# Performance work log

Hardware: AMD Instinct MI355X
Metric: run time of the kernel (lower is better)

The kernel has to match this reference:

```python
import jax, jax.numpy as jnp
import numpy as np

N = 2
GRIDS = [(512, 512), (256, 256), (128, 128), (64, 64), (32, 32)]
STRIDES = [4, 8, 16, 32, 64]
SIZES = [32, 64, 128, 256, 512]
ASPECTS = (0.5, 1.0, 2.0)
A = len(ASPECTS)
IMG_H = IMG_W = 2048
PRE_NMS = 1000      # pre_nms_top_n['testing']
POST_NMS = 1000     # post_nms_top_n['testing']
NMS_THRESH = 0.7
SCORE_THRESH = 0.0
MIN_SIZE = 1e-3
BBOX_XFORM_CLIP = float(np.log(1000.0 / 16.0))  # torchvision BoxCoder clamp


def _make_anchors():
    """AnchorGenerator.grid_anchors for each level; returns list of [H*W*A, 4]."""
    ar = jnp.asarray(ASPECTS, jnp.float32)
    hr = jnp.sqrt(ar)
    wr = 1.0 / hr
    levels = []
    for (gh, gw), s, size in zip(GRIDS, STRIDES, SIZES):
        ws = wr * size
        hs = hr * size
        base = jnp.round(jnp.stack([-ws, -hs, ws, hs], 1) / 2.0)  # [A,4]
        sx = (jnp.arange(gw) * s).astype(jnp.float32)
        sy = (jnp.arange(gh) * s).astype(jnp.float32)
        yy, xx = jnp.meshgrid(sy, sx, indexing='ij')
        shifts = jnp.stack([xx.ravel(), yy.ravel(), xx.ravel(), yy.ravel()], 1)
        levels.append((shifts[:, None, :] + base[None, :, :]).reshape(-1, 4))
    return levels


def _flatten_obj(o):
    # permute_and_flatten with C=1: [N,A,H,W] -> [N, H*W*A]
    n, ac, h, w = o.shape
    return o.reshape(n, ac, 1, h, w).transpose(0, 3, 4, 1, 2).reshape(n, -1)


def _flatten_box(b):
    # permute_and_flatten with C=4: [N,A*4,H,W] -> [N, H*W*A, 4]
    n, a4, h, w = b.shape
    return b.reshape(n, a4 // 4, 4, h, w).transpose(0, 3, 4, 1, 2).reshape(n, -1, 4)


def _decode(deltas, anchors):
    # BoxCoder.decode with weights (1,1,1,1); deltas [N,M,4], anchors [M,4]
    wa = anchors[:, 2] - anchors[:, 0]
    ha = anchors[:, 3] - anchors[:, 1]
    cxa = anchors[:, 0] + 0.5 * wa
    cya = anchors[:, 1] + 0.5 * ha
    dx, dy = deltas[..., 0], deltas[..., 1]
    dw = jnp.minimum(deltas[..., 2], BBOX_XFORM_CLIP)
    dh = jnp.minimum(deltas[..., 3], BBOX_XFORM_CLIP)
    cx = dx * wa + cxa
    cy = dy * ha + cya
    w = jnp.exp(dw) * wa
    h = jnp.exp(dh) * ha
    return jnp.stack([cx - 0.5 * w, cy - 0.5 * h, cx + 0.5 * w, cy + 0.5 * h], -1)


def _nms_select(boxes, scores, n_out, thresh):
    """Greedy NMS returning fixed n_out (index, valid) pairs. boxes [K,4]."""
    area = jnp.maximum(boxes[:, 2] - boxes[:, 0], 0.0) * jnp.maximum(boxes[:, 3] - boxes[:, 1], 0.0)

    def step(s, _):
        i = jnp.argmax(s)
        valid = s[i] > -jnp.inf
        b = boxes[i]
        lt = jnp.maximum(boxes[:, :2], b[:2])
        rb = jnp.minimum(boxes[:, 2:], b[2:])
        wh = jnp.maximum(rb - lt, 0.0)
        inter = wh[:, 0] * wh[:, 1]
        iou = inter / (area + area[i] - inter + 1e-9)
        s = jnp.where(iou > thresh, -jnp.inf, s).at[i].set(-jnp.inf)
        return s, (i, valid)

    _, (idx, valid) = jax.lax.scan(step, scores, None, length=n_out)
    return idx, valid


def _rpn_forward(objs, dts):
    anchors = _make_anchors()
    b_all, s_all, l_all = [], [], []
    for li, (o, d, a) in enumerate(zip(objs, dts, anchors)):
        of = _flatten_obj(o)            # [N, HWA]
        df = _flatten_box(d)            # [N, HWA, 4]
        props = _decode(df, a)          # [N, HWA, 4]
        k = min(PRE_NMS, of.shape[1])
        ts, ti = jax.lax.top_k(of, k)   # top-k on raw objectness (per level)
        b_all.append(jnp.take_along_axis(props, ti[..., None], 1))
        s_all.append(ts)
        l_all.append(jnp.full((of.shape[0], k), float(li), jnp.float32))
    boxes = jnp.concatenate(b_all, 1)   # [N, K, 4]
    raw = jnp.concatenate(s_all, 1)     # [N, K]
    lvl = jnp.concatenate(l_all, 1)     # [N, K]

    def per_image(bx, rs, lv):
        sc = jax.nn.sigmoid(rs)
        x1 = jnp.clip(bx[:, 0], 0.0, IMG_W)
        y1 = jnp.clip(bx[:, 1], 0.0, IMG_H)
        x2 = jnp.clip(bx[:, 2], 0.0, IMG_W)
        y2 = jnp.clip(bx[:, 3], 0.0, IMG_H)
        bx = jnp.stack([x1, y1, x2, y2], 1)
        keep = ((x2 - x1) >= MIN_SIZE) & ((y2 - y1) >= MIN_SIZE) & (sc > SCORE_THRESH)
        ms = jnp.where(keep, sc, -jnp.inf)
        off = lv * (IMG_W + IMG_H + 1.0)  # batched_nms level offset
        idx, valid = _nms_select(jax.lax.stop_gradient(bx + off[:, None]),
                                 jax.lax.stop_gradient(ms), POST_NMS, NMS_THRESH)
        v = valid.astype(bx.dtype)
        ob = bx[idx] * v[:, None]
        os = sc[idx] * v
        return jnp.concatenate([ob, os[:, None]], 1)  # [POST_NMS, 5]

    return jax.vmap(per_image)(boxes, raw, lvl)       # [N, POST_NMS, 5]


def setup_inputs() -> dict:
    key = jax.random.key(0)
    ks = jax.random.split(key, 10)
    inp = {}
    for i, (gh, gw) in enumerate(GRIDS):
        inp[f"obj{i}"] = jax.random.normal(ks[i], (N, A, gh, gw), jnp.float32)
        inp[f"box{i}"] = jax.random.normal(ks[5 + i], (N, A * 4, gh, gw), jnp.float32) * 0.5
    return inp


def reference(obj0, obj1, obj2, obj3, obj4, box0, box1, box2, box3, box4):
    return _rpn_forward([obj0, obj1, obj2, obj3, obj4],
                        [box0, box1, box2, box3, box4])
```

## Files before the change

kernel.cpp:

```cpp
#include <hip/hip_runtime.h>
#include <cmath>

#pragma clang fp contract(off)

typedef unsigned int u32;
typedef unsigned short u16;
typedef unsigned long long u64;

#define K_PER_LVL 1000
#define KTOT 5000
#define NIMG 2
#define BINS 16384
#define BIN_SHIFT 18
#define SEGW (BINS / 256)
#define EQ_CAP 2048
#define ECAP 32768
#define LECAP 24576
#define CBUF 1024
#define RNK_IB 512
#define RNK_JB 250
#define RNK_NJ (KTOT / RNK_JB)

__constant__ int c_LG[5] = {512, 256, 128, 64, 32};
__constant__ int c_LS[5] = {4, 8, 16, 32, 64};
__constant__ int c_LZ[5] = {32, 64, 128, 256, 512};
__constant__ int c_LM[5] = {786432, 196608, 49152, 12288, 3072};

struct Ptrs { const float* o[5]; const float* b[5]; };

__device__ inline u32 fkey(float f) {
    u32 u = __float_as_uint(f);
    return (u & 0x80000000u) ? ~u : (u | 0x80000000u);
}

__global__ __launch_bounds__(256) void k_zero(u32* __restrict__ z, int nwords) {
    int i = blockIdx.x * 256 + threadIdx.x;
    int stride = gridDim.x * 256;
    for (; i < nwords; i += stride) z[i] = 0;
}

__global__ __launch_bounds__(256) void k_hist(Ptrs P, u32* __restrict__ hist) {
    int p = blockIdx.y; int l = p % 5; int n = p / 5;
    int M4 = c_LM[l] >> 2;
    const float4* base = (const float4*)(P.o[l] + (size_t)n * c_LM[l]);
    __shared__ u32 lh[BINS];
    for (int i = threadIdx.x; i < BINS; i += 256) lh[i] = 0;
    __syncthreads();
    int stride = gridDim.x * 256;
    for (int i = blockIdx.x * 256 + threadIdx.x; i < M4; i += stride) {
        float4 v = base[i];
        atomicAdd(&lh[fkey(v.x) >> BIN_SHIFT], 1u);
        atomicAdd(&lh[fkey(v.y) >> BIN_SHIFT], 1u);
        atomicAdd(&lh[fkey(v.z) >> BIN_SHIFT], 1u);
        atomicAdd(&lh[fkey(v.w) >> BIN_SHIFT], 1u);
    }
    __syncthreads();
    for (int i = threadIdx.x; i < BINS; i += 256) {
        u32 c = lh[i];
        if (c) atomicAdd(&hist[p * BINS + i], c);
    }
}

__global__ __launch_bounds__(256) void k_resolve(const u32* __restrict__ hist,
                                                 int* __restrict__ binB, int* __restrict__ kneed,
                                                 int* __restrict__ g0) {
    int p = blockIdx.x, t = threadIdx.x;
    __shared__ u32 seg[256];
    __shared__ u32 tail[SEGW];
    __shared__ int sgS; __shared__ u32 GS;
    u32 s = 0;
    const u32* hb = hist + p * BINS;
    int base = t * SEGW;
    for (int q = 0; q < SEGW; ++q) s += hb[base + q];
    seg[t] = s;
    __syncthreads();
    if (t == 0) {
        u32 G = 0; int sg = 255;
        for (; sg > 0; --sg) {
            if (G + seg[sg] >= (u32)K_PER_LVL) break;
            G += seg[sg];
        }
        sgS = sg; GS = G;
    }
    __syncthreads();
    int sg = sgS;
    if (t < SEGW) tail[t] = hb[sg * SEGW + t];
    __syncthreads();
    if (t == 0) {
        u32 G = GS; int B = sg * SEGW;
        for (int b = SEGW - 1; b >= 0; --b) {
            u32 c = tail[b];
            if (G + c >= (u32)K_PER_LVL) { B = sg * SEGW + b; break; }
            G += c;
        }
        binB[p] = B;
        kneed[p] = K_PER_LVL - (int)G;
        g0[p] = (int)G;
    }
}

__global__ __launch_bounds__(256) void k_compact(Ptrs P, const int* __restrict__ binB,
                                                 u32* gcnt, u32* ecnt,
                                                 int* __restrict__ sel, u64* __restrict__ eq) {
    int p = blockIdx.y; int l = p % 5; int n = p / 5;
    int M4 = c_LM[l] >> 2; int gg = c_LM[l] / 3;
    const float4* base = (const float4*)(P.o[l] + (size_t)n * c_LM[l]);
    int B = binB[p];
    __shared__ u32 lsel[CBUF];
    __shared__ u64 leq[CBUF];
    __shared__ u32 cSel, cEq, baseSel, baseEq;
    if (threadIdx.x == 0) { cSel = 0; cEq = 0; }
    __syncthreads();
    int stride = gridDim.x * 256;
    for (int i4 = blockIdx.x * 256 + threadIdx.x; i4 < M4; i4 += stride) {
        float4 v = base[i4];
        float vv[4] = {v.x, v.y, v.z, v.w};
        #pragma unroll
        for (int q = 0; q < 4; ++q) {
            u32 k = fkey(vv[q]);
            int bin = (int)(k >> BIN_SHIFT);
            if (bin < B) continue;
            int i = i4 * 4 + q;
            int a = i / gg; int pix = i - a * gg; int m = pix * 3 + a;
            if (bin > B) {
                u32 t = atomicAdd(&cSel, 1u);
                if (t < CBUF) lsel[t] = (u32)m;
                else { u32 pos = atomicAdd(&gcnt[p], 1u); sel[p * K_PER_LVL + pos] = m; }
            } else {
                u64 pk = ((u64)k << 20) | (u64)(0xFFFFFu ^ (u32)m);
                u32 t = atomicAdd(&cEq, 1u);
                if (t < CBUF) leq[t] = pk;
                else { u32 e = atomicAdd(&ecnt[p], 1u); if (e < EQ_CAP) eq[(size_t)p * EQ_CAP + e] = pk; }
            }
        }
    }
    __syncthreads();
    if (threadIdx.x == 0) {
        u32 ns = cSel < CBUF ? cSel : CBUF;
        u32 ne = cEq < CBUF ? cEq : CBUF;
        baseSel = ns ? atomicAdd(&gcnt[p], ns) : 0u;
        baseEq  = ne ? atomicAdd(&ecnt[p], ne) : 0u;
    }
    __syncthreads();
    u32 ns = cSel < CBUF ? cSel : CBUF;
    u32 ne = cEq < CBUF ? cEq : CBUF;
    for (u32 i = threadIdx.x; i < ns; i += 256) sel[p * K_PER_LVL + baseSel + i] = (int)lsel[i];
    for (u32 i = threadIdx.x; i < ne; i += 256) {
        u32 slot = baseEq + i;
        if (slot < EQ_CAP) eq[(size_t)p * EQ_CAP + slot] = leq[i];
    }
}

__global__ __launch_bounds__(256) void k_eqsel(const u32* __restrict__ ecnt, const int* __restrict__ kneed,
                                               const int* __restrict__ g0,
                                               const u64* __restrict__ eq, int* __restrict__ sel) {
    int p = blockIdx.x, t = threadIdx.x;
    int E = (int)ecnt[p]; if (E > EQ_CAP) E = EQ_CAP;
    int KF = kneed[p]; int G0 = g0[p];
    __shared__ u64 a[EQ_CAP];
    for (int i = t; i < E; i += 256) a[i] = eq[(size_t)p * EQ_CAP + i];
    __syncthreads();
    u64 mine[8]; int rk[8];
    #pragma unroll
    for (int q = 0; q < 8; ++q) {
        int i = t + q * 256;
        mine[q] = (i < E) ? a[i] : 0ULL;
        rk[q] = 0;
    }
    for (int j = 0; j < E; ++j) {
        u64 v = a[j];
        #pragma unroll
        for (int q = 0; q < 8; ++q) rk[q] += (v > mine[q]) ? 1 : 0;
    }
    #pragma unroll
    for (int q = 0; q < 8; ++q) {
        int i = t + q * 256;
        if (i < E && rk[q] < KF) {
            int m = (int)(0xFFFFFu ^ (u32)(mine[q] & 0xFFFFFu));
            sel[p * K_PER_LVL + G0 + rk[q]] = m;
        }
    }
}

__global__ void k_feat(Ptrs P, const int* __restrict__ sel, u64* __restrict__ key64,
                       float* __restrict__ csc, float* __restrict__ cbox, float* __restrict__ cobox) {
    int tid = blockIdx.x * 256 + threadIdx.x;
    if (tid >= NIMG * KTOT) return;
    int p = tid / K_PER_LVL, s = tid - p * K_PER_LVL;
    int n = p / 5, l = p % 5;
    int G = c_LG[l], S = c_LS[l], Z = c_LZ[l];
    int gg = G * G;
    int m = sel[p * K_PER_LVL + s];
    int a = m % 3; int pix = m / 3; int h = pix / G; int w = pix - h * G;

    const float ars[3] = {0.5f, 1.0f, 2.0f};
    float ar = ars[a];
    float hr = sqrtf(ar), wr = 1.0f / hr;
    float wsz = wr * (float)Z, hsz = hr * (float)Z;
    float bx1 = rintf(-0.5f * wsz), by1 = rintf(-0.5f * hsz);
    float bx2 = rintf(0.5f * wsz),  by2 = rintf(0.5f * hsz);
    float sx = (float)(w * S), sy = (float)(h * S);
    float ax1 = sx + bx1, ay1 = sy + by1, ax2 = sx + bx2, ay2 = sy + by2;
    float wa = ax2 - ax1, ha = ay2 - ay1;
    float cxa = ax1 + 0.5f * wa, cya = ay1 + 0.5f * ha;

    const float* bb = P.b[l] + (size_t)n * 12 * gg;
    float dx = bb[(a * 4 + 0) * gg + pix];
    float dy = bb[(a * 4 + 1) * gg + pix];
    const float CLIPV = 4.135166556742356f;
    float dw = fminf(bb[(a * 4 + 2) * gg + pix], CLIPV);
    float dh = fminf(bb[(a * 4 + 3) * gg + pix], CLIPV);
    float cx = dx * wa + cxa, cy = dy * ha + cya;
    float ww = expf(dw) * wa, hh = expf(dh) * ha;
    float x1 = cx - 0.5f * ww, y1 = cy - 0.5f * hh;
    float x2 = cx + 0.5f * ww, y2 = cy + 0.5f * hh;
    x1 = fminf(fmaxf(x1, 0.f), 2048.f);
    y1 = fminf(fmaxf(y1, 0.f), 2048.f);
    x2 = fminf(fmaxf(x2, 0.f), 2048.f);
    y2 = fminf(fmaxf(y2, 0.f), 2048.f);

    float raw = P.o[l][(size_t)n * 3 * gg + a * gg + pix];
    float sc = 1.0f / (1.0f + expf(-raw));
    bool keep = (x2 - x1 >= 1e-3f) && (y2 - y1 >= 1e-3f) && (sc > 0.0f);

    int slot = n * KTOT + l * K_PER_LVL + s;
    u32 tb = ((u32)l << 20) | (u32)m;
    u32 kk = keep ? fkey(raw) : 0u;
    key64[slot] = ((u64)kk << 23) | (u64)(tb ^ 0x7FFFFFu);

    csc[slot] = keep ? sc : -INFINITY;
    cbox[slot * 4 + 0] = x1; cbox[slot * 4 + 1] = y1;
    cbox[slot * 4 + 2] = x2; cbox[slot * 4 + 3] = y2;
    float off = 4097.0f * (float)l;
    cobox[slot * 4 + 0] = x1 + off; cobox[slot * 4 + 1] = y1 + off;
    cobox[slot * 4 + 2] = x2 + off; cobox[slot * 4 + 3] = y2 + off;
}

__global__ __launch_bounds__(256) void k_rankp(const u64* __restrict__ key64, u32* __restrict__ rpart) {
    int n = blockIdx.z;
    int i0 = blockIdx.x * RNK_IB;
    int j0 = blockIdx.y * RNK_JB;
    __shared__ u64 kj[RNK_JB];
    const u64* kb = key64 + (size_t)n * KTOT;
    for (int t = threadIdx.x; t < RNK_JB; t += 256) kj[t] = kb[j0 + t];
    __syncthreads();
    int i1 = i0 + threadIdx.x, i2 = i1 + 256;
    u64 k1 = (i1 < KTOT) ? kb[i1] : ~0ULL;
    u64 k2 = (i2 < KTOT) ? kb[i2] : ~0ULL;
    u32 r1 = 0, r2 = 0;
    #pragma unroll 10
    for (int j = 0; j < RNK_JB; ++j) {
        u64 v = kj[j];
        r1 += (v > k1) ? 1u : 0u;
        r2 += (v > k2) ? 1u : 0u;
    }
    u32* rp = rpart + (size_t)blockIdx.y * (NIMG * KTOT) + n * KTOT;
    if (i1 < KTOT) rp[i1] = r1;
    if (i2 < KTOT) rp[i2] = r2;
}

__global__ __launch_bounds__(256) void k_scat(const u32* __restrict__ rpart, const float* __restrict__ csc,
                       const float* __restrict__ cbox, const float* __restrict__ cobox,
                       float* __restrict__ ssc, float* __restrict__ sbox, float* __restrict__ sobox) {
    int n = blockIdx.y;
    int i = blockIdx.x * 256 + threadIdx.x;
    if (i >= KTOT) return;
    int idx = n * KTOT + i;
    u32 rank = 0;
    #pragma unroll
    for (int jb = 0; jb < RNK_NJ; ++jb) rank += rpart[(size_t)jb * (NIMG * KTOT) + idx];
    int src = idx, dst = n * KTOT + (int)rank;
    ssc[dst] = csc[src];
    sbox[dst * 4 + 0] = cbox[src * 4 + 0]; sbox[dst * 4 + 1] = cbox[src * 4 + 1];
    sbox[dst * 4 + 2] = cbox[src * 4 + 2]; sbox[dst * 4 + 3] = cbox[src * 4 + 3];
    sobox[dst * 4 + 0] = cobox[src * 4 + 0]; sobox[dst * 4 + 1] = cobox[src * 4 + 1];
    sobox[dst * 4 + 2] = cobox[src * 4 + 2]; sobox[dst * 4 + 3] = cobox[src * 4 + 3];
}

__global__ void k_edge(const float* __restrict__ sobox, u32* __restrict__ gE, u32* __restrict__ gPairs) {
    int n = blockIdx.z;
    int bi = blockIdx.x, bj = blockIdx.y;
    if (bj < bi) return;
    int i = bi * 64 + threadIdx.x;
    int j0 = bj * 64;
    __shared__ float cb[64][4];
    int jl = j0 + threadIdx.x;
    if (jl < KTOT) {
        cb[threadIdx.x][0] = sobox[(size_t)(n * KTOT + jl) * 4 + 0];
        cb[threadIdx.x][1] = sobox[(size_t)(n * KTOT + jl) * 4 + 1];
        cb[threadIdx.x][2] = sobox[(size_t)(n * KTOT + jl) * 4 + 2];
        cb[threadIdx.x][3] = sobox[(size_t)(n * KTOT + jl) * 4 + 3];
    } else {
        cb[threadIdx.x][0] = 0.f; cb[threadIdx.x][1] = 0.f;
        cb[threadIdx.x][2] = 0.f; cb[threadIdx.x][3] = 0.f;
    }
    __syncthreads();
    if (i >= KTOT) return;
    float x1 = sobox[(size_t)(n * KTOT + i) * 4 + 0];
    float y1 = sobox[(size_t)(n * KTOT + i) * 4 + 1];
    float x2 = sobox[(size_t)(n * KTOT + i) * 4 + 2];
    float y2 = sobox[(size_t)(n * KTOT + i) * 4 + 3];
    float areai = fmaxf(x2 - x1, 0.f) * fmaxf(y2 - y1, 0.f);
    int lim = KTOT - j0; if (lim > 64) lim = 64;
    for (int jj = 0; jj < lim; ++jj) {
        int j = j0 + jj;
        if (j <= i) continue;
        float bx1 = cb[jj][0], by1 = cb[jj][1], bx2 = cb[jj][2], by2 = cb[jj][3];
        float areaj = fmaxf(bx2 - bx1, 0.f) * fmaxf(by2 - by1, 0.f);
        float ltx = fmaxf(x1, bx1), lty = fmaxf(y1, by1);
        float rbx = fminf(x2, bx2), rby = fminf(y2, by2);
        float iw = fmaxf(rbx - ltx, 0.f), ih = fmaxf(rby - lty, 0.f);
        float inter = iw * ih;
        float iou = inter / (areai + areaj - inter + 1e-9f);
        if (iou > 0.7f) {
            u32 pos = atomicAdd(&gE[n], 1u);
            if (pos < ECAP) gPairs[(size_t)n * ECAP + pos] = ((u32)i << 13) | (u32)j;
        }
    }
}

__global__ __launch_bounds__(256, 1) void k_nms(const float* __restrict__ ssc,
                      const float* __restrict__ sbox,
                      const u32* __restrict__ gE, const u32* __restrict__ gPairs,
                      u16* __restrict__ gEdges, float* __restrict__ out) {
    int n = blockIdx.x, tid = threadIdx.x;
    int lane = tid & 63, wv = tid >> 6;
    __shared__ u32 cnt[KTOT];
    __shared__ u32 offs[KTOT + 1];
    __shared__ u16 edges[LECAP];
    __shared__ u32 rem32[160];
    __shared__ u32 colLo[64], colHi[64];
    __shared__ u32 scanb[256];
    __shared__ int picksS;

    for (int i = tid; i < KTOT; i += 256) cnt[i] = 0;
    if (tid < 160) rem32[tid] = 0xFFFFFFFFu;
    __syncthreads();
    for (int w = wv; w < 79; w += 4) {
        int i = w * 64 + lane;
        bool dead = (i >= KTOT) || !(ssc[n * KTOT + i] > -INFINITY);
        u64 db = __ballot(dead);
        if (lane == 0) { rem32[2 * w] = (u32)db; rem32[2 * w + 1] = (u32)(db >> 32); }
    }
    __syncthreads();

    int E = (int)gE[n]; if (E > ECAP) E = ECAP;
    for (int k = tid; k < E; k += 256) {
        u32 p = gPairs[(size_t)n * ECAP + k];
        atomicAdd(&cnt[p >> 13], 1u);
    }
    __syncthreads();
    u32 s = 0; int base = tid * 20;
    if (tid < 250) for (int q = 0; q < 20; ++q) s += cnt[base + q];
    scanb[tid] = s;
    __syncthreads();
    for (int off = 1; off < 256; off <<= 1) {
        u32 v = (tid >= off) ? scanb[tid - off] : 0;
        __syncthreads();
        scanb[tid] += v;
        __syncthreads();
    }
    u32 tbase = (tid == 0) ? 0u : scanb[tid - 1];
    if (tid < 250) {
        u32 run = tbase;
        for (int q = 0; q < 20; ++q) { offs[base + q] = run; run += cnt[base + q]; }
    }
    if (tid == 0) offs[KTOT] = scanb[255];
    __syncthreads();
    for (int i = tid; i < KTOT; i += 256) cnt[i] = 0;
    __syncthreads();
    for (int k = tid; k < E; k += 256) {
        u32 p = gPairs[(size_t)n * ECAP + k];
        u32 src = p >> 13, dst = p & 0x1FFFu;
        u32 slot = offs[src] + atomicAdd(&cnt[src], 1u);
        if (slot < LECAP) edges[slot] = (u16)dst;
        else gEdges[(size_t)n * ECAP + slot] = (u16)dst;
    }
    __syncthreads();

    if (wv == 0) {
        int picks = 0;
        for (int w = 0; w < 79 && picks < 1000; ++w) {
            u64 rw = ((u64)rem32[2 * w + 1] << 32) | rem32[2 * w];
            u64 alive = ~rw;
            if (alive == 0ULL) continue;
            int c = w * 64 + lane;
            bool amAlive = ((alive >> lane) & 1ULL) != 0ULL;
            int e0 = 0, e1 = 0;
            if (amAlive) { e0 = (int)offs[c]; e1 = (int)offs[c + 1]; }
            colLo[lane] = 0; colHi[lane] = 0;
            bool anyIntra = false;
            for (int k = e0; k < e1; ++k) {
                int dst = (k < LECAP) ? (int)edges[k] : (int)gEdges[(size_t)n * ECAP + k];
                if ((dst >> 6) == w) {
                    if (lane < 32) atomicOr(&colLo[dst & 63], 1u << lane);
                    else           atomicOr(&colHi[dst & 63], 1u << (lane - 32));
                    anyIntra = true;
                }
            }
            u64 cm;
            if (__ballot(anyIntra) == 0ULL) {
                cm = alive;
            } else {
                u64 col = ((u64)colHi[lane] << 32) | colLo[lane];
                cm = 0ULL;
                for (int e = 0; e < 64; ++e) {
                    if (!((alive >> e) & 1ULL)) continue;
                    u64 ce = __shfl(col, e);
                    if ((cm & ce) == 0ULL) cm |= (1ULL << e);
                }
            }
            int allowed = 1000 - picks;
            int ncom = __popcll(cm);
            while (ncom > allowed) { cm &= ~(1ULL << (63 - __clzll(cm))); --ncom; }
            if ((cm >> lane) & 1ULL) {
                int pos = picks + (int)__popcll(cm & ((1ULL << lane) - 1ULL));
                const float* bp = &sbox[(size_t)(n * KTOT + c) * 4];
                float* op = &out[(n * 1000 + pos) * 5];
                op[0] = bp[0]; op[1] = bp[1]; op[2] = bp[2]; op[3] = bp[3];
                op[4] = ssc[n * KTOT + c];
                for (int k = e0; k < e1; ++k) {
                    int dst = (k < LECAP) ? (int)edges[k] : (int)gEdges[(size_t)n * ECAP + k];
                    atomicOr(&rem32[dst >> 5], 1u << (dst & 31));
                }
            }
            picks += ncom;
        }
        if (lane == 0) picksS = picks;
    }
    __syncthreads();
    int picksF = picksS;
    int basec = (n * 1000 + picksF) * 5, cntz = (1000 - picksF) * 5;
    for (int t = tid; t < cntz; t += 256) out[basec + t] = 0.f;
}

constexpr size_t OFF_HIST   = 0;
constexpr size_t OFF_GCNT   = OFF_HIST + 10 * BINS * 4;
constexpr size_t OFF_ECNT   = OFF_GCNT + 64;
constexpr size_t OFF_GEC    = OFF_ECNT + 64;
constexpr size_t ZERO_WORDS = (10 * BINS * 4 + 192) / 4;
constexpr size_t OFF_BINB   = OFF_GEC + 64;
constexpr size_t OFF_KNEED  = OFF_BINB + 64;
constexpr size_t OFF_G0     = OFF_KNEED + 64;
constexpr size_t OFF_SEL    = OFF_G0 + 64;
constexpr size_t OFF_EQ     = OFF_SEL + 10 * K_PER_LVL * 4;
constexpr size_t OFF_KEY64  = OFF_EQ + (size_t)10 * EQ_CAP * 8;
constexpr size_t OFF_CSC    = OFF_KEY64 + (size_t)NIMG * KTOT * 8;
constexpr size_t OFF_CBOX   = OFF_CSC + (size_t)NIMG * KTOT * 4;
constexpr size_t OFF_COBOX  = OFF_CBOX + (size_t)NIMG * KTOT * 16;
constexpr size_t OFF_SSC    = OFF_COBOX + (size_t)NIMG * KTOT * 16;
constexpr size_t OFF_SBOX   = OFF_SSC + (size_t)NIMG * KTOT * 4;
constexpr size_t OFF_SOBOX  = OFF_SBOX + (size_t)NIMG * KTOT * 16;
constexpr size_t OFF_PAIRS  = OFF_SOBOX + (size_t)NIMG * KTOT * 16;
constexpr size_t OFF_ESPILL = OFF_PAIRS + (size_t)NIMG * ECAP * 4;
constexpr size_t OFF_RPART  = OFF_ESPILL + (size_t)NIMG * ECAP * 2;
constexpr size_t WS_NEEDED  = OFF_RPART + (size_t)RNK_NJ * NIMG * KTOT * 4;

extern "C" void kernel_launch(void* const* d_in, const int* in_sizes, int n_in,
                              void* d_out, int out_size, void* d_ws, size_t ws_size,
                              hipStream_t stream) {
    if (ws_size < WS_NEEDED) return;

    bool dictOrder = (in_sizes[1] > in_sizes[0]);
    Ptrs P;
    for (int l = 0; l < 5; ++l) {
        P.o[l] = (const float*)d_in[dictOrder ? (2 * l)     : l];
        P.b[l] = (const float*)d_in[dictOrder ? (2 * l + 1) : (5 + l)];
    }
    char* ws = (char*)d_ws;
    u32*   hist   = (u32*)(ws + OFF_HIST);
    u32*   gcnt   = (u32*)(ws + OFF_GCNT);
    u32*   ecnt   = (u32*)(ws + OFF_ECNT);
    u32*   gec    = (u32*)(ws + OFF_GEC);
    int*   binB   = (int*)(ws + OFF_BINB);
    int*   kneed  = (int*)(ws + OFF_KNEED);
    int*   g0     = (int*)(ws + OFF_G0);
    int*   sel    = (int*)(ws + OFF_SEL);
    u64*   eq     = (u64*)(ws + OFF_EQ);
    u64*   key64  = (u64*)(ws + OFF_KEY64);
    float* csc    = (float*)(ws + OFF_CSC);
    float* cbox   = (float*)(ws + OFF_CBOX);
    float* cobox  = (float*)(ws + OFF_COBOX);
    float* ssc    = (float*)(ws + OFF_SSC);
    float* sbox   = (float*)(ws + OFF_SBOX);
    float* sobox  = (float*)(ws + OFF_SOBOX);
    u32*   pairs  = (u32*)(ws + OFF_PAIRS);
    u16*   espill = (u16*)(ws + OFF_ESPILL);
    u32*   rpart  = (u32*)(ws + OFF_RPART);
    float* out    = (float*)d_out;

    k_zero<<<dim3(64), 256, 0, stream>>>(hist, (int)ZERO_WORDS);
    k_hist<<<dim3(32, 10), 256, 0, stream>>>(P, hist);
    k_resolve<<<10, 256, 0, stream>>>(hist, binB, kneed, g0);
    k_compact<<<dim3(64, 10), 256, 0, stream>>>(P, binB, gcnt, ecnt, sel, eq);
    k_eqsel<<<10, 256, 0, stream>>>(ecnt, kneed, g0, eq, sel);
    k_feat<<<dim3((NIMG * KTOT + 255) / 256), 256, 0, stream>>>(P, sel, key64, csc, cbox, cobox);
    k_rankp<<<dim3((KTOT + RNK_IB - 1) / RNK_IB, RNK_NJ, NIMG), 256, 0, stream>>>(key64, rpart);
    k_scat<<<dim3((KTOT + 255) / 256, NIMG), 256, 0, stream>>>(rpart, csc, cbox, cobox, ssc, sbox, sobox);
    k_edge<<<dim3(79, 79, NIMG), 64, 0, stream>>>(sobox, gec, pairs);
    k_nms<<<NIMG, 256, 0, stream>>>(ssc, sbox, gec, pairs, espill, out);
}
```

Before: 204.4 us.

## Compute IoU edges on unsorted boxes concurrently with rank, remap via rank in NMS

The IoU edge search now runs on the unsorted candidate boxes and shares one launch with the partial rank counting, so it no longer has to wait for the sort and scatter. The scatter kernel stops writing sorted offset boxes and instead records each candidate's rank. NMS uses that rank to turn each pair into a (higher-ranked, lower-ranked) sorted-index edge. This removes a kernel launch, a serial dependency and a scatter buffer, at the cost of two extra global rank lookups per edge inside NMS and a tile-index decode loop in the merged kernel.

```diff
diff --git a/kernel.cpp b/kernel.cpp
--- a/kernel.cpp
+++ b/kernel.cpp
@@ -20,6 +20,8 @@
 #define RNK_IB 512
 #define RNK_JB 250
 #define RNK_NJ (KTOT / RNK_JB)
+#define RNK_TILES 200
+#define EDGE_TILES 820
 
 __constant__ int c_LG[5] = {512, 256, 128, 64, 32};
 __constant__ int c_LS[5] = {4, 8, 16, 32, 64};
@@ -236,70 +238,57 @@
     cobox[slot * 4 + 2] = x2 + off; cobox[slot * 4 + 3] = y2 + off;
 }
 
-__global__ __launch_bounds__(256) void k_rankp(const u64* __restrict__ key64, u32* __restrict__ rpart) {
-    int n = blockIdx.z;
-    int i0 = blockIdx.x * RNK_IB;
-    int j0 = blockIdx.y * RNK_JB;
+__global__ __launch_bounds__(256) void k_redge(const u64* __restrict__ key64, u32* __restrict__ rpart,
+                                               const float* __restrict__ cobox,
+                                               u32* __restrict__ gE, u32* __restrict__ gPairs) {
+    int n = blockIdx.y;
+    int x = blockIdx.x;
     __shared__ u64 kj[RNK_JB];
-    const u64* kb = key64 + (size_t)n * KTOT;
-    for (int t = threadIdx.x; t < RNK_JB; t += 256) kj[t] = kb[j0 + t];
-    __syncthreads();
-    int i1 = i0 + threadIdx.x, i2 = i1 + 256;
-    u64 k1 = (i1 < KTOT) ? kb[i1] : ~0ULL;
-    u64 k2 = (i2 < KTOT) ? kb[i2] : ~0ULL;
-    u32 r1 = 0, r2 = 0;
-    #pragma unroll 10
-    for (int j = 0; j < RNK_JB; ++j) {
-        u64 v = kj[j];
-        r1 += (v > k1) ? 1u : 0u;
-        r2 += (v > k2) ? 1u : 0u;
-    }
-    u32* rp = rpart + (size_t)blockIdx.y * (NIMG * KTOT) + n * KTOT;
-    if (i1 < KTOT) rp[i1] = r1;
-    if (i2 < KTOT) rp[i2] = r2;
-}
-
-__global__ __launch_bounds__(256) void k_scat(const u32* __restrict__ rpart, const float* __restrict__ csc,
-                       const float* __restrict__ cbox, const float* __restrict__ cobox,
-                       float* __restrict__ ssc, float* __restrict__ sbox, float* __restrict__ sobox) {
-    int n = blockIdx.y;
-    int i = blockIdx.x * 256 + threadIdx.x;
+    __shared__ float cb[64][4];
+    if (x < RNK_TILES) {
+        int i0 = (x / 20) * RNK_IB;
+        int j0 = (x % 20) * RNK_JB;
+        const u64* kb = key64 + (size_t)n * KTOT;
+        for (int t = threadIdx.x; t < RNK_JB; t += 256) kj[t] = kb[j0 + t];
+        __syncthreads();
+        int i1 = i0 + threadIdx.x, i2 = i1 + 256;
+        u64 k1 = (i1 < KTOT) ? kb[i1] : ~0ULL;
+        u64 k2 = (i2 < KTOT) ? kb[i2] : ~0ULL;
+        u32 r1 = 0, r2 = 0;
+        #pragma unroll 10
+        for (int j = 0; j < RNK_JB; ++j) {
+            u64 v = kj[j];
+            r1 += (v > k1) ? 1u : 0u;
+            r2 += (v > k2) ? 1u : 0u;
+        }
+        u32* rp = rpart + (size_t)(x % 20) * (NIMG * KTOT) + n * KTOT;
+        if (i1 < KTOT) rp[i1] = r1;
+        if (i2 < KTOT) rp[i2] = r2;
+        return;
+    }
+    int e = x - RNK_TILES, bi = 0;
+    while (true) { int c = 79 - 4 * bi; if (e < c) break; e -= c; ++bi; }
+    int bj = 4 * bi + e;
+    int i = bi * 256 + threadIdx.x;
+    int j0 = bj * 64;
+    if (threadIdx.x < 64) {
+        int jl = j0 + threadIdx.x;
+        if (jl < KTOT) {
+            cb[threadIdx.x][0] = cobox[(size_t)(n * KTOT + jl) * 4 + 0];
+            cb[threadIdx.x][1] = cobox[(size_t)(n * KTOT + jl) * 4 + 1];
+            cb[threadIdx.x][2] = cobox[(size_t)(n * KTOT + jl) * 4 + 2];
+            cb[threadIdx.x][3] = cobox[(size_t)(n * KTOT + jl) * 4 + 3];
+        } else {
+            cb[threadIdx.x][0] = 0.f; cb[threadIdx.x][1] = 0.f;
+            cb[threadIdx.x][2] = 0.f; cb[threadIdx.x][3] = 0.f;
+        }
+    }
+    __syncthreads();
     if (i >= KTOT) return;
-    int idx = n * KTOT + i;
-    u32 rank = 0;
-    #pragma unroll
-    for (int jb = 0; jb < RNK_NJ; ++jb) rank += rpart[(size_t)jb * (NIMG * KTOT) + idx];
-    int src = idx, dst = n * KTOT + (int)rank;
-    ssc[dst] = csc[src];
-    sbox[dst * 4 + 0] = cbox[src * 4 + 0]; sbox[dst * 4 + 1] = cbox[src * 4 + 1];
-    sbox[dst * 4 + 2] = cbox[src * 4 + 2]; sbox[dst * 4 + 3] = cbox[src * 4 + 3];
-    sobox[dst * 4 + 0] = cobox[src * 4 + 0]; sobox[dst * 4 + 1] = cobox[src * 4 + 1];
-    sobox[dst * 4 + 2] = cobox[src * 4 + 2]; sobox[dst * 4 + 3] = cobox[src * 4 + 3];
-}
-
-__global__ void k_edge(const float* __restrict__ sobox, u32* __restrict__ gE, u32* __restrict__ gPairs) {
-    int n = blockIdx.z;
-    int bi = blockIdx.x, bj = blockIdx.y;
-    if (bj < bi) return;
-    int i = bi * 64 + threadIdx.x;
-    int j0 = bj * 64;
-    __shared__ float cb[64][4];
-    int jl = j0 + threadIdx.x;
-    if (jl < KTOT) {
-        cb[threadIdx.x][0] = sobox[(size_t)(n * KTOT + jl) * 4 + 0];
-        cb[threadIdx.x][1] = sobox[(size_t)(n * KTOT + jl) * 4 + 1];
-        cb[threadIdx.x][2] = sobox[(size_t)(n * KTOT + jl) * 4 + 2];
-        cb[threadIdx.x][3] = sobox[(size_t)(n * KTOT + jl) * 4 + 3];
-    } else {
-        cb[threadIdx.x][0] = 0.f; cb[threadIdx.x][1] = 0.f;
-        cb[threadIdx.x][2] = 0.f; cb[threadIdx.x][3] = 0.f;
-    }
-    __syncthreads();
-    if (i >= KTOT) return;
-    float x1 = sobox[(size_t)(n * KTOT + i) * 4 + 0];
-    float y1 = sobox[(size_t)(n * KTOT + i) * 4 + 1];
-    float x2 = sobox[(size_t)(n * KTOT + i) * 4 + 2];
-    float y2 = sobox[(size_t)(n * KTOT + i) * 4 + 3];
+    float x1 = cobox[(size_t)(n * KTOT + i) * 4 + 0];
+    float y1 = cobox[(size_t)(n * KTOT + i) * 4 + 1];
+    float x2 = cobox[(size_t)(n * KTOT + i) * 4 + 2];
+    float y2 = cobox[(size_t)(n * KTOT + i) * 4 + 3];
     float areai = fmaxf(x2 - x1, 0.f) * fmaxf(y2 - y1, 0.f);
     int lim = KTOT - j0; if (lim > 64) lim = 64;
     for (int jj = 0; jj < lim; ++jj) {
@@ -319,8 +308,25 @@
     }
 }
 
+__global__ __launch_bounds__(256) void k_scat(const u32* __restrict__ rpart, const float* __restrict__ csc,
+                       const float* __restrict__ cbox,
+                       float* __restrict__ ssc, float* __restrict__ sbox, u32* __restrict__ rankArr) {
+    int n = blockIdx.y;
+    int i = blockIdx.x * 256 + threadIdx.x;
+    if (i >= KTOT) return;
+    int idx = n * KTOT + i;
+    u32 rank = 0;
+    #pragma unroll
+    for (int jb = 0; jb < RNK_NJ; ++jb) rank += rpart[(size_t)jb * (NIMG * KTOT) + idx];
+    rankArr[idx] = rank;
+    int src = idx, dst = n * KTOT + (int)rank;
+    ssc[dst] = csc[src];
+    sbox[dst * 4 + 0] = cbox[src * 4 + 0]; sbox[dst * 4 + 1] = cbox[src * 4 + 1];
+    sbox[dst * 4 + 2] = cbox[src * 4 + 2]; sbox[dst * 4 + 3] = cbox[src * 4 + 3];
+}
+
 __global__ __launch_bounds__(256, 1) void k_nms(const float* __restrict__ ssc,
-                      const float* __restrict__ sbox,
+                      const float* __restrict__ sbox, const u32* __restrict__ rankArr,
                       const u32* __restrict__ gE, const u32* __restrict__ gPairs,
                       u16* __restrict__ gEdges, float* __restrict__ out) {
     int n = blockIdx.x, tid = threadIdx.x;
@@ -347,7 +353,9 @@
     int E = (int)gE[n]; if (E > ECAP) E = ECAP;
     for (int k = tid; k < E; k += 256) {
         u32 p = gPairs[(size_t)n * ECAP + k];
-        atomicAdd(&cnt[p >> 13], 1u);
+        u32 ra = rankArr[n * KTOT + (p >> 13)], rb = rankArr[n * KTOT + (p & 0x1FFFu)];
+        u32 src = ra < rb ? ra : rb;
+        atomicAdd(&cnt[src], 1u);
     }
     __syncthreads();
     u32 s = 0; int base = tid * 20;
@@ -371,7 +379,8 @@
     __syncthreads();
     for (int k = tid; k < E; k += 256) {
         u32 p = gPairs[(size_t)n * ECAP + k];
-        u32 src = p >> 13, dst = p & 0x1FFFu;
+        u32 ra = rankArr[n * KTOT + (p >> 13)], rb = rankArr[n * KTOT + (p & 0x1FFFu)];
+        u32 src = ra < rb ? ra : rb, dst = ra < rb ? rb : ra;
         u32 slot = offs[src] + atomicAdd(&cnt[src], 1u);
         if (slot < LECAP) edges[slot] = (u16)dst;
         else gEdges[(size_t)n * ECAP + slot] = (u16)dst;
@@ -450,8 +459,8 @@
 constexpr size_t OFF_COBOX  = OFF_CBOX + (size_t)NIMG * KTOT * 16;
 constexpr size_t OFF_SSC    = OFF_COBOX + (size_t)NIMG * KTOT * 16;
 constexpr size_t OFF_SBOX   = OFF_SSC + (size_t)NIMG * KTOT * 4;
-constexpr size_t OFF_SOBOX  = OFF_SBOX + (size_t)NIMG * KTOT * 16;
-constexpr size_t OFF_PAIRS  = OFF_SOBOX + (size_t)NIMG * KTOT * 16;
+constexpr size_t OFF_RANK   = OFF_SBOX + (size_t)NIMG * KTOT * 16;
+constexpr size_t OFF_PAIRS  = OFF_RANK + (size_t)NIMG * KTOT * 4;
 constexpr size_t OFF_ESPILL = OFF_PAIRS + (size_t)NIMG * ECAP * 4;
 constexpr size_t OFF_RPART  = OFF_ESPILL + (size_t)NIMG * ECAP * 2;
 constexpr size_t WS_NEEDED  = OFF_RPART + (size_t)RNK_NJ * NIMG * KTOT * 4;
@@ -483,7 +492,7 @@
     float* cobox  = (float*)(ws + OFF_COBOX);
     float* ssc    = (float*)(ws + OFF_SSC);
     float* sbox   = (float*)(ws + OFF_SBOX);
-    float* sobox  = (float*)(ws + OFF_SOBOX);
+    u32*   rankA  = (u32*)(ws + OFF_RANK);
     u32*   pairs  = (u32*)(ws + OFF_PAIRS);
     u16*   espill = (u16*)(ws + OFF_ESPILL);
     u32*   rpart  = (u32*)(ws + OFF_RPART);
@@ -495,8 +504,7 @@
     k_compact<<<dim3(64, 10), 256, 0, stream>>>(P, binB, gcnt, ecnt, sel, eq);
     k_eqsel<<<10, 256, 0, stream>>>(ecnt, kneed, g0, eq, sel);
     k_feat<<<dim3((NIMG * KTOT + 255) / 256), 256, 0, stream>>>(P, sel, key64, csc, cbox, cobox);
-    k_rankp<<<dim3((KTOT + RNK_IB - 1) / RNK_IB, RNK_NJ, NIMG), 256, 0, stream>>>(key64, rpart);
-    k_scat<<<dim3((KTOT + 255) / 256, NIMG), 256, 0, stream>>>(rpart, csc, cbox, cobox, ssc, sbox, sobox);
-    k_edge<<<dim3(79, 79, NIMG), 64, 0, stream>>>(sobox, gec, pairs);
-    k_nms<<<NIMG, 256, 0, stream>>>(ssc, sbox, gec, pairs, espill, out);
-}
+    k_redge<<<dim3(RNK_TILES + EDGE_TILES, NIMG), 256, 0, stream>>>(key64, rpart, cobox, gec, pairs);
+    k_scat<<<dim3((KTOT + 255) / 256, NIMG), 256, 0, stream>>>(rpart, csc, cbox, ssc, sbox, rankA);
+    k_nms<<<NIMG, 256, 0, stream>>>(ssc, sbox, rankA, gec, pairs, espill, out);
+}
```

Result: faster. 198.3 us (-3.0%).
